# Performance work log

Measured on AMD Instinct MI355X. Metric: run time of the kernel, lower is better.

Reference implementation:

```python
import jax, jax.numpy as jnp
import numpy as np

NUM_GRAPHS = 64


def gcn_conv(x, edge_index, W, b):
    # PyG GCNConv: x' = D^-1/2 (A+I) D^-1/2 (x W) + b, self-loops added.
    n = x.shape[0]
    h = x @ W  # [N, out]
    loop = jnp.arange(n)
    src = jnp.concatenate([edge_index[0], loop])
    dst = jnp.concatenate([edge_index[1], loop])
    deg = jax.ops.segment_sum(jnp.ones_like(dst, dtype=h.dtype), dst, num_segments=n)
    dinv = jnp.where(deg > 0, jax.lax.rsqrt(deg), 0.0)
    norm = dinv[src] * dinv[dst]  # [E+N]
    msgs = h[src] * norm[:, None]  # gather + scale
    out = jax.ops.segment_sum(msgs, dst, num_segments=n)  # scatter-add
    return out + b


def lstm_step(x, W_ih, W_hh, b_ih, b_hh):
    # single time step, zero initial state; PyTorch gate order i,f,g,o
    H = W_hh.shape[1]
    gates = x @ W_ih.T + b_ih + b_hh  # h0 = 0 so W_hh term vanishes
    i, f, g, o = jnp.split(gates, 4, axis=-1)
    i, f, o = jax.nn.sigmoid(i), jax.nn.sigmoid(f), jax.nn.sigmoid(o)
    c = i * jnp.tanh(g)  # f * c0 = 0
    return o * jnp.tanh(c)


def setup_inputs() -> dict:
    key = jax.random.key(0)
    ks = jax.random.split(key, 16)
    N, E, F, G, H, C = 50000, 600000, 128, 128, 256, 1
    s = lambda *sh: 1.0 / np.sqrt(sh[-1])
    return {
        "x": jax.random.normal(ks[0], (N, F), jnp.float32),
        "edge_index": jax.random.randint(ks[1], (2, E), 0, N),
        "batch": jnp.sort(jax.random.randint(ks[2], (N,), 0, NUM_GRAPHS)),
        "W1": jax.random.normal(ks[3], (F, G), jnp.float32) * s(F, G),
        "b1": jnp.zeros((G,), jnp.float32),
        "W2": jax.random.normal(ks[4], (G, G), jnp.float32) * s(G, G),
        "b2": jnp.zeros((G,), jnp.float32),
        "W_ih": jax.random.normal(ks[5], (4 * H, G), jnp.float32) * s(4 * H, G),
        "W_hh": jax.random.normal(ks[6], (4 * H, H), jnp.float32) * s(4 * H, H),
        "b_ih": jnp.zeros((4 * H,), jnp.float32),
        "b_hh": jnp.zeros((4 * H,), jnp.float32),
        "Wm": jax.random.normal(ks[7], (C, H), jnp.float32) * s(C, H),
        "bm": jnp.zeros((C,), jnp.float32),
        "Wv": jax.random.normal(ks[8], (C, H), jnp.float32) * s(C, H),
        "bv": jnp.zeros((C,), jnp.float32),
    }


def reference(x, edge_index, batch, W1, b1, W2, b2, W_ih, W_hh, b_ih, b_hh, Wm, bm, Wv, bv):
    h = jax.nn.relu(gcn_conv(x, edge_index, W1, b1))
    h = jax.nn.relu(gcn_conv(h, edge_index, W2, b2))
    # global mean pool over graphs
    sums = jax.ops.segment_sum(h, batch, num_segments=NUM_GRAPHS)
    cnts = jax.ops.segment_sum(jnp.ones_like(batch, dtype=h.dtype), batch, num_segments=NUM_GRAPHS)
    pooled = sums / jnp.maximum(cnts, 1.0)[:, None]  # [G_graphs, gcn_hidden]
    hT = lstm_step(pooled, W_ih, W_hh, b_ih, b_hh)  # [G_graphs, lstm_hidden]
    mean = hT @ Wm.T + bm
    log_var = jax.nn.softplus(hT @ Wv.T + bv)
    return (mean, log_var)
```

## Files before the change

### kernel.cpp

```cpp
#include <hip/hip_runtime.h>
#include <hip/hip_bf16.h>
#include <math.h>


#define POOL_SUB 32

typedef __attribute__((ext_vector_type(8))) short bf16x8;
typedef __attribute__((ext_vector_type(4))) float f32x4;

static __device__ __forceinline__ unsigned short f2bf(float f) {
    union { float f; unsigned int u; } v; v.f = f;
    unsigned int u = v.u;
    unsigned int r = u + 0x7FFFu + ((u >> 16) & 1u);
    return (unsigned short)(r >> 16);
}
static __device__ __forceinline__ unsigned int pack2bf(float lo, float hi) {
    return (unsigned int)f2bf(lo) | ((unsigned int)f2bf(hi) << 16);
}
static __device__ __forceinline__ float bflo(unsigned int v) {
    union { unsigned int u; float f; } w; w.u = v << 16; return w.f;
}
static __device__ __forceinline__ float bfhi(unsigned int v) {
    union { unsigned int u; float f; } w; w.u = v & 0xFFFF0000u; return w.f;
}
static __device__ __forceinline__ bf16x8 f8_to_bf(float4 f0, float4 f1) {
    union { unsigned int u[4]; bf16x8 v; } r;
    r.u[0] = pack2bf(f0.x, f0.y);
    r.u[1] = pack2bf(f0.z, f0.w);
    r.u[2] = pack2bf(f1.x, f1.y);
    r.u[3] = pack2bf(f1.z, f1.w);
    return r.v;
}

__global__ void zero_kernel(int* __restrict__ p, int n) {
    int i = blockIdx.x * blockDim.x + threadIdx.x;
    if (i < n) p[i] = 0;
}

__global__ void count_deg_kernel(const int* __restrict__ dst, int E, int* __restrict__ deg) {
    int e = blockIdx.x * blockDim.x + threadIdx.x;
    if (e < E) atomicAdd(&deg[dst[e]], 1);
}

__global__ void scan_pass1(const int* __restrict__ deg, int n,
                           int* __restrict__ rowptr, int* __restrict__ bsums) {
    __shared__ int s[256];
    int tid = threadIdx.x;
    int base = blockIdx.x * 1024;
    int v[4];
    int mysum = 0;
#pragma unroll
    for (int j = 0; j < 4; ++j) {
        int idx = base + tid * 4 + j;
        v[j] = (idx < n) ? deg[idx] : 0;
        mysum += v[j];
    }
    s[tid] = mysum;
    __syncthreads();
    for (int off = 1; off < 256; off <<= 1) {
        int t = (tid >= off) ? s[tid - off] : 0;
        __syncthreads();
        s[tid] += t;
        __syncthreads();
    }
    int excl = s[tid] - mysum;
#pragma unroll
    for (int j = 0; j < 4; ++j) {
        int idx = base + tid * 4 + j;
        if (idx < n) rowptr[idx] = excl;
        excl += v[j];
    }
    if (tid == 255) bsums[blockIdx.x] = s[255];
}

__global__ void scan_pass2(int* bsums, int nb) {
    __shared__ int s[64];
    int tid = threadIdx.x;
    int v = (tid < nb) ? bsums[tid] : 0;
    s[tid] = v;
    __syncthreads();
    for (int off = 1; off < 64; off <<= 1) {
        int t = (tid >= off) ? s[tid - off] : 0;
        __syncthreads();
        s[tid] += t;
        __syncthreads();
    }
    if (tid < nb) bsums[tid] = s[tid] - v;
    if (tid == 63) bsums[nb] = s[63];
}

__global__ void scan_pass3(int* __restrict__ rowptr, const int* __restrict__ bsums,
                           const int* __restrict__ deg, float* __restrict__ dinv,
                           int n, int nb) {
    int tid = threadIdx.x;
    int base = blockIdx.x * 1024;
    int add = bsums[blockIdx.x];
#pragma unroll
    for (int j = 0; j < 4; ++j) {
        int idx = base + tid * 4 + j;
        if (idx < n) {
            rowptr[idx] += add;
            dinv[idx] = rsqrtf((float)deg[idx] + 1.0f);
        }
    }
    if (blockIdx.x == 0 && tid == 0) rowptr[n] = bsums[nb];
}

__global__ void fill_csr_kernel(const int* __restrict__ src, const int* __restrict__ dst, int E,
                                const int* __restrict__ rowptr, int* __restrict__ cursor,
                                int* __restrict__ csr) {
    int e = blockIdx.x * blockDim.x + threadIdx.x;
    if (e < E) {
        int d = dst[e];
        int pos = rowptr[d] + atomicAdd(&cursor[d], 1);
        csr[pos] = src[e];
    }
}

__global__ void wcvt_kernel(const float* __restrict__ W1, const float* __restrict__ W2,
                            unsigned short* __restrict__ Wt1, unsigned short* __restrict__ Wt2) {
    int nb = blockIdx.x & 127;
    const float* Ws = (blockIdx.x < 128) ? W1 : W2;
    unsigned short* Wd = (blockIdx.x < 128) ? Wt1 : Wt2;
    int k = threadIdx.x;
    Wd[nb * 128 + k] = f2bf(Ws[(size_t)k * 128 + nb]);
}

__global__ __launch_bounds__(256) void gemm_mfma_f32a_kernel(const float* __restrict__ A,
                                                             const unsigned short* __restrict__ Wt,
                                                             const float* __restrict__ dinv,
                                                             unsigned short* __restrict__ out,
                                                             int n) {
    int tid = threadIdx.x;
    int l = tid & 63;
    int wid = tid >> 6;
    int rowbase = blockIdx.x * 64 + wid * 16;
    int lc = l & 15;
    int kq = l >> 4;

    int arow = rowbase + lc; if (arow > n - 1) arow = n - 1;
    const float* Ap = A + (size_t)arow * 128 + kq * 8;
    const unsigned short* Wp = Wt + (size_t)lc * 128 + kq * 8;

    f32x4 acc[8];
#pragma unroll
    for (int c = 0; c < 8; ++c) acc[c] = (f32x4){0.f, 0.f, 0.f, 0.f};

#pragma unroll
    for (int ks = 0; ks < 4; ++ks) {
        float4 f0 = *(const float4*)(Ap + ks * 32);
        float4 f1 = *(const float4*)(Ap + ks * 32 + 4);
        bf16x8 a = f8_to_bf(f0, f1);
#pragma unroll
        for (int c = 0; c < 8; ++c) {
            bf16x8 b = *(const bf16x8*)(Wp + c * 2048 + ks * 32);
            acc[c] = __builtin_amdgcn_mfma_f32_16x16x32_bf16(a, b, acc[c], 0, 0, 0);
        }
    }

    int r0 = kq * 4;
    float s[4];
    int orow[4];
#pragma unroll
    for (int r = 0; r < 4; ++r) {
        orow[r] = rowbase + r0 + r;
        s[r] = (orow[r] < n) ? dinv[orow[r]] : 0.f;
    }
#pragma unroll
    for (int c = 0; c < 8; ++c) {
#pragma unroll
        for (int r = 0; r < 4; ++r) {
            if (orow[r] < n)
                out[(size_t)orow[r] * 128 + c * 16 + lc] = f2bf(acc[c][r] * s[r]);
        }
    }
}

__global__ __launch_bounds__(256) void gemm_mfma_kernel(const unsigned short* __restrict__ A,
                                                        const unsigned short* __restrict__ Wt,
                                                        const float* __restrict__ dinv,
                                                        unsigned short* __restrict__ out,
                                                        int n) {
    int tid = threadIdx.x;
    int l = tid & 63;
    int wid = tid >> 6;
    int rowbase = blockIdx.x * 64 + wid * 16;
    int lc = l & 15;
    int kq = l >> 4;

    int arow = rowbase + lc; if (arow > n - 1) arow = n - 1;
    const unsigned short* Ap = A + (size_t)arow * 128 + kq * 8;
    const unsigned short* Wp = Wt + (size_t)lc * 128 + kq * 8;

    f32x4 acc[8];
#pragma unroll
    for (int c = 0; c < 8; ++c) acc[c] = (f32x4){0.f, 0.f, 0.f, 0.f};

#pragma unroll
    for (int ks = 0; ks < 4; ++ks) {
        bf16x8 a = *(const bf16x8*)(Ap + ks * 32);
#pragma unroll
        for (int c = 0; c < 8; ++c) {
            bf16x8 b = *(const bf16x8*)(Wp + c * 2048 + ks * 32);
            acc[c] = __builtin_amdgcn_mfma_f32_16x16x32_bf16(a, b, acc[c], 0, 0, 0);
        }
    }

    int r0 = kq * 4;
    float s[4];
    int orow[4];
#pragma unroll
    for (int r = 0; r < 4; ++r) {
        orow[r] = rowbase + r0 + r;
        s[r] = (orow[r] < n) ? dinv[orow[r]] : 0.f;
    }
#pragma unroll
    for (int c = 0; c < 8; ++c) {
#pragma unroll
        for (int r = 0; r < 4; ++r) {
            if (orow[r] < n)
                out[(size_t)orow[r] * 128 + c * 16 + lc] = f2bf(acc[c][r] * s[r]);
        }
    }
}

__global__ __launch_bounds__(256) void aggregate_kernel(const unsigned int* __restrict__ g,
                                                        const int* __restrict__ rowptr,
                                                        const int* __restrict__ csr,
                                                        const float* __restrict__ dinv,
                                                        const float* __restrict__ bias,
                                                        unsigned int* __restrict__ out, int n) {
    int lane = threadIdx.x & 63;
    int node = (blockIdx.x * blockDim.x + threadIdx.x) >> 6;
    if (node >= n) return;
    int beg = rowptr[node], end = rowptr[node + 1];
    unsigned int sv = g[(size_t)node * 64 + lane];
    float ax = bflo(sv), ay = bfhi(sv);
    int e = beg;
    for (; e + 4 <= end; e += 4) {
        int s0 = csr[e + 0], s1 = csr[e + 1], s2 = csr[e + 2], s3 = csr[e + 3];
        unsigned int v0 = g[(size_t)s0 * 64 + lane];
        unsigned int v1 = g[(size_t)s1 * 64 + lane];
        unsigned int v2 = g[(size_t)s2 * 64 + lane];
        unsigned int v3 = g[(size_t)s3 * 64 + lane];
        ax += bflo(v0) + bflo(v1) + bflo(v2) + bflo(v3);
        ay += bfhi(v0) + bfhi(v1) + bfhi(v2) + bfhi(v3);
    }
    for (; e < end; ++e) {
        unsigned int v0 = g[(size_t)csr[e] * 64 + lane];
        ax += bflo(v0);
        ay += bfhi(v0);
    }
    float dv = dinv[node];
    float2 b = ((const float2*)bias)[lane];
    float rx = fmaxf(dv * ax + b.x, 0.f);
    float ry = fmaxf(dv * ay + b.y, 0.f);
    out[(size_t)node * 64 + lane] = pack2bf(rx, ry);
}

__global__ __launch_bounds__(64) void pool_partial_kernel(const unsigned int* __restrict__ h,
                                                          const int* __restrict__ batch, int n,
                                                          float* __restrict__ partial) {
    int g = blockIdx.x / POOL_SUB;
    int sub = blockIdx.x % POOL_SUB;
    int t = threadIdx.x;
    int lo = 0, hi = n;
    while (lo < hi) { int mid = (lo + hi) >> 1; if (batch[mid] < g) lo = mid + 1; else hi = mid; }
    int start = lo;
    hi = n;
    while (lo < hi) { int mid = (lo + hi) >> 1; if (batch[mid] < g + 1) lo = mid + 1; else hi = mid; }
    int end = lo;
    int len = end - start;
    int b0 = start + (int)((long long)len * sub / POOL_SUB);
    int b1 = start + (int)((long long)len * (sub + 1) / POOL_SUB);
    float ax = 0.f, ay = 0.f;
    int i = b0;
    for (; i + 4 <= b1; i += 4) {
        unsigned int v0 = h[(size_t)(i + 0) * 64 + t];
        unsigned int v1 = h[(size_t)(i + 1) * 64 + t];
        unsigned int v2 = h[(size_t)(i + 2) * 64 + t];
        unsigned int v3 = h[(size_t)(i + 3) * 64 + t];
        ax += bflo(v0) + bflo(v1) + bflo(v2) + bflo(v3);
        ay += bfhi(v0) + bfhi(v1) + bfhi(v2) + bfhi(v3);
    }
    for (; i < b1; ++i) {
        unsigned int v0 = h[(size_t)i * 64 + t];
        ax += bflo(v0);
        ay += bfhi(v0);
    }
    partial[(size_t)blockIdx.x * 128 + 2 * t]     = ax;
    partial[(size_t)blockIdx.x * 128 + 2 * t + 1] = ay;
}

__global__ __launch_bounds__(256) void pool_lstm_kernel(const float* __restrict__ partial,
                                                        const int* __restrict__ batch, int n,
                                                        const float* __restrict__ W_ih,
                                                        const float* __restrict__ b_ih,
                                                        const float* __restrict__ b_hh,
                                                        const float* __restrict__ Wm,
                                                        const float* __restrict__ bm,
                                                        const float* __restrict__ Wv,
                                                        const float* __restrict__ bv,
                                                        float* __restrict__ out) {
    __shared__ __align__(16) float p[128];
    __shared__ float redm[256];
    __shared__ float redv[256];
    int gph = blockIdx.x;
    int tid = threadIdx.x;
    if (tid < 128) {
        int lo = 0, hi = n;
        while (lo < hi) { int mid = (lo + hi) >> 1; if (batch[mid] < gph) lo = mid + 1; else hi = mid; }
        int start = lo;
        hi = n;
        while (lo < hi) { int mid = (lo + hi) >> 1; if (batch[mid] < gph + 1) lo = mid + 1; else hi = mid; }
        int end = lo;
        float acc = 0.f;
#pragma unroll
        for (int s = 0; s < POOL_SUB; ++s)
            acc += partial[(size_t)(gph * POOL_SUB + s) * 128 + tid];
        p[tid] = acc / fmaxf((float)(end - start), 1.0f);
    }
    __syncthreads();
    float gi = b_ih[tid] + b_hh[tid];
    float gg = b_ih[512 + tid] + b_hh[512 + tid];
    float go = b_ih[768 + tid] + b_hh[768 + tid];
    const float4* wi = (const float4*)(W_ih + (size_t)tid * 128);
    const float4* wg = (const float4*)(W_ih + (size_t)(512 + tid) * 128);
    const float4* wo = (const float4*)(W_ih + (size_t)(768 + tid) * 128);
    const float4* p4 = (const float4*)p;
#pragma unroll 8
    for (int k = 0; k < 32; ++k) {
        float4 xv = p4[k];
        float4 a = wi[k], bq = wg[k], cq = wo[k];
        gi += xv.x * a.x + xv.y * a.y + xv.z * a.z + xv.w * a.w;
        gg += xv.x * bq.x + xv.y * bq.y + xv.z * bq.z + xv.w * bq.w;
        go += xv.x * cq.x + xv.y * cq.y + xv.z * cq.z + xv.w * cq.w;
    }
    float iv = 1.f / (1.f + expf(-gi));
    float cv = iv * tanhf(gg);
    float ov = 1.f / (1.f + expf(-go));
    float hT = ov * tanhf(cv);
    redm[tid] = hT * Wm[tid];
    redv[tid] = hT * Wv[tid];
    __syncthreads();
    for (int s = 128; s > 0; s >>= 1) {
        if (tid < s) { redm[tid] += redm[tid + s]; redv[tid] += redv[tid + s]; }
        __syncthreads();
    }
    if (tid == 0) {
        out[gph] = redm[0] + bm[0];
        float xv = redv[0] + bv[0];
        out[64 + gph] = fmaxf(xv, 0.f) + log1pf(expf(-fabsf(xv)));
    }
}

extern "C" void kernel_launch(void* const* d_in, const int* in_sizes, int n_in,
                              void* d_out, int out_size, void* d_ws, size_t ws_size,
                              hipStream_t stream) {
    const float* x     = (const float*)d_in[0];
    const int*   edge  = (const int*)d_in[1];
    const int*   batch = (const int*)d_in[2];
    const float* W1    = (const float*)d_in[3];
    const float* b1    = (const float*)d_in[4];
    const float* W2    = (const float*)d_in[5];
    const float* b2    = (const float*)d_in[6];
    const float* W_ih  = (const float*)d_in[7];
    const float* b_ih  = (const float*)d_in[9];
    const float* b_hh  = (const float*)d_in[10];
    const float* Wm    = (const float*)d_in[11];
    const float* bm    = (const float*)d_in[12];
    const float* Wv    = (const float*)d_in[13];
    const float* bv    = (const float*)d_in[14];
    float* out = (float*)d_out;

    const int N = in_sizes[0] / 128;
    const int E = in_sizes[1] / 2;
    const int* srcIdx = edge;
    const int* dstIdx = edge + E;

    char* ws = (char*)d_ws;
    size_t off = 0;
    const size_t gB = (size_t)N * 64 * sizeof(unsigned int);
    unsigned int* gbuf = (unsigned int*)(ws + off); off += gB;
    unsigned int* hbuf = (unsigned int*)(ws + off); off += gB;
    int* deg    = (int*)(ws + off);   off += (size_t)N * sizeof(int);
    int* cursor = (int*)(ws + off);   off += (size_t)N * sizeof(int);
    int* rowptr = (int*)(ws + off);   off += (size_t)(N + 1) * sizeof(int);
    off = (off + 255) & ~(size_t)255;
    int* bsums  = (int*)(ws + off);   off += 512;
    int* csr    = (int*)(ws + off);   off += (size_t)E * sizeof(int);
    off = (off + 255) & ~(size_t)255;
    float* dinv = (float*)(ws + off); off += (size_t)N * sizeof(float);
    off = (off + 255) & ~(size_t)255;
    unsigned short* Wt1 = (unsigned short*)(ws + off); off += 128 * 128 * sizeof(unsigned short);
    unsigned short* Wt2 = (unsigned short*)(ws + off); off += 128 * 128 * sizeof(unsigned short);
    off = (off + 255) & ~(size_t)255;
    float* partial = (float*)(ws + off); off += (size_t)64 * POOL_SUB * 128 * sizeof(float);

    zero_kernel<<<(2 * N + 255) / 256, 256, 0, stream>>>(deg, 2 * N);

    wcvt_kernel<<<256, 128, 0, stream>>>(W1, W2, Wt1, Wt2);

    int eb = (E + 255) / 256;
    count_deg_kernel<<<eb, 256, 0, stream>>>(dstIdx, E, deg);

    int nb = (N + 1023) / 1024;
    scan_pass1<<<nb, 256, 0, stream>>>(deg, N, rowptr, bsums);
    scan_pass2<<<1, 64, 0, stream>>>(bsums, nb);
    scan_pass3<<<nb, 256, 0, stream>>>(rowptr, bsums, deg, dinv, N, nb);
    fill_csr_kernel<<<eb, 256, 0, stream>>>(srcIdx, dstIdx, E, rowptr, cursor, csr);

    int gb = (N + 63) / 64;
    int ab = (N + 3) / 4;

    gemm_mfma_f32a_kernel<<<gb, 256, 0, stream>>>(x, Wt1, dinv, (unsigned short*)gbuf, N);
    aggregate_kernel<<<ab, 256, 0, stream>>>(gbuf, rowptr, csr, dinv, b1, hbuf, N);
    gemm_mfma_kernel<<<gb, 256, 0, stream>>>((const unsigned short*)hbuf, Wt2, dinv, (unsigned short*)gbuf, N);
    aggregate_kernel<<<ab, 256, 0, stream>>>(gbuf, rowptr, csr, dinv, b2, hbuf, N);

    pool_partial_kernel<<<64 * POOL_SUB, 64, 0, stream>>>(hbuf, batch, N, partial);
    pool_lstm_kernel<<<64, 256, 0, stream>>>(partial, batch, N, W_ih, b_ih, b_hh, Wm, bm, Wv, bv, out);
}
```

Before: 222.3 us.

## Split GCN aggregation into feature-slice passes and fuse small setup kernels

The aggregation kernel now processes the 128 features in four pass-major slices, with each wave gathering four edges at once into 16-lane groups and reducing via cross-lane shuffles. This is meant to shrink the gathered working set per pass so it stays cache-resident and to raise memory parallelism. Separately, zeroing and weight conversion are merged into one kernel, and the second and third scan passes are merged, to cut launch count. The cost is 4x redundant reads of rowptr/csr and narrower 64-byte gather segments.

```diff
diff --git a/kernel.cpp b/kernel.cpp
--- a/kernel.cpp
+++ b/kernel.cpp
@@ -32,9 +32,21 @@
     return r.v;
 }
 
-__global__ void zero_kernel(int* __restrict__ p, int n) {
-    int i = blockIdx.x * blockDim.x + threadIdx.x;
-    if (i < n) p[i] = 0;
+__global__ __launch_bounds__(256) void prep_kernel(int* __restrict__ zp, int zwords,
+                                                   const float* __restrict__ W1,
+                                                   const float* __restrict__ W2,
+                                                   unsigned short* __restrict__ Wt1,
+                                                   unsigned short* __restrict__ Wt2, int zb) {
+    int b = blockIdx.x;
+    int t = threadIdx.x;
+    if (b < zb) {
+        int i = b * 256 + t;
+        if (i < zwords) zp[i] = 0;
+    } else {
+        int col = b - zb;
+        if (t < 128) Wt1[col * 128 + t] = f2bf(W1[(size_t)t * 128 + col]);
+        else { int k = t - 128; Wt2[col * 128 + k] = f2bf(W2[(size_t)k * 128 + col]); }
+    }
 }
 
 __global__ void count_deg_kernel(const int* __restrict__ dst, int E, int* __restrict__ deg) {
@@ -73,28 +85,23 @@
     if (tid == 255) bsums[blockIdx.x] = s[255];
 }
 
-__global__ void scan_pass2(int* bsums, int nb) {
-    __shared__ int s[64];
+__global__ void scan_pass23(int* __restrict__ rowptr, const int* __restrict__ bsums,
+                            const int* __restrict__ deg, float* __restrict__ dinv,
+                            int n, int nb) {
+    __shared__ int sm[64];
+    __shared__ int pref[65];
     int tid = threadIdx.x;
-    int v = (tid < nb) ? bsums[tid] : 0;
-    s[tid] = v;
+    if (tid < 64) sm[tid] = (tid < nb) ? bsums[tid] : 0;
     __syncthreads();
-    for (int off = 1; off < 64; off <<= 1) {
-        int t = (tid >= off) ? s[tid - off] : 0;
-        __syncthreads();
-        s[tid] += t;
-        __syncthreads();
-    }
-    if (tid < nb) bsums[tid] = s[tid] - v;
-    if (tid == 63) bsums[nb] = s[63];
-}
-
-__global__ void scan_pass3(int* __restrict__ rowptr, const int* __restrict__ bsums,
-                           const int* __restrict__ deg, float* __restrict__ dinv,
-                           int n, int nb) {
-    int tid = threadIdx.x;
+    if (tid == 0) {
+        int s = 0;
+#pragma unroll 8
+        for (int i = 0; i < 64; ++i) { pref[i] = s; s += sm[i]; }
+        pref[64] = s;
+    }
+    __syncthreads();
+    int add = pref[blockIdx.x];
     int base = blockIdx.x * 1024;
-    int add = bsums[blockIdx.x];
 #pragma unroll
     for (int j = 0; j < 4; ++j) {
         int idx = base + tid * 4 + j;
@@ -103,7 +110,7 @@
             dinv[idx] = rsqrtf((float)deg[idx] + 1.0f);
         }
     }
-    if (blockIdx.x == 0 && tid == 0) rowptr[n] = bsums[nb];
+    if (blockIdx.x == 0 && tid == 0) rowptr[n] = pref[64];
 }
 
 __global__ void fill_csr_kernel(const int* __restrict__ src, const int* __restrict__ dst, int E,
@@ -115,15 +122,6 @@
         int pos = rowptr[d] + atomicAdd(&cursor[d], 1);
         csr[pos] = src[e];
     }
-}
-
-__global__ void wcvt_kernel(const float* __restrict__ W1, const float* __restrict__ W2,
-                            unsigned short* __restrict__ Wt1, unsigned short* __restrict__ Wt2) {
-    int nb = blockIdx.x & 127;
-    const float* Ws = (blockIdx.x < 128) ? W1 : W2;
-    unsigned short* Wd = (blockIdx.x < 128) ? Wt1 : Wt2;
-    int k = threadIdx.x;
-    Wd[nb * 128 + k] = f2bf(Ws[(size_t)k * 128 + nb]);
 }
 
 __global__ __launch_bounds__(256) void gemm_mfma_f32a_kernel(const float* __restrict__ A,
@@ -229,33 +227,37 @@
                                                         const int* __restrict__ csr,
                                                         const float* __restrict__ dinv,
                                                         const float* __restrict__ bias,
-                                                        unsigned int* __restrict__ out, int n) {
+                                                        unsigned int* __restrict__ out,
+                                                        int n, int npb) {
+    int pass = blockIdx.x / npb;
+    int blk  = blockIdx.x % npb;
     int lane = threadIdx.x & 63;
-    int node = (blockIdx.x * blockDim.x + threadIdx.x) >> 6;
+    int wid  = threadIdx.x >> 6;
+    int node = blk * 4 + wid;
     if (node >= n) return;
+    int li = lane & 15, sub = lane >> 4;
+    int base = pass * 16;
     int beg = rowptr[node], end = rowptr[node + 1];
-    unsigned int sv = g[(size_t)node * 64 + lane];
-    float ax = bflo(sv), ay = bfhi(sv);
+    float ax = 0.f, ay = 0.f;
     int e = beg;
     for (; e + 4 <= end; e += 4) {
-        int s0 = csr[e + 0], s1 = csr[e + 1], s2 = csr[e + 2], s3 = csr[e + 3];
-        unsigned int v0 = g[(size_t)s0 * 64 + lane];
-        unsigned int v1 = g[(size_t)s1 * 64 + lane];
-        unsigned int v2 = g[(size_t)s2 * 64 + lane];
-        unsigned int v3 = g[(size_t)s3 * 64 + lane];
-        ax += bflo(v0) + bflo(v1) + bflo(v2) + bflo(v3);
-        ay += bfhi(v0) + bfhi(v1) + bfhi(v2) + bfhi(v3);
-    }
-    for (; e < end; ++e) {
-        unsigned int v0 = g[(size_t)csr[e] * 64 + lane];
-        ax += bflo(v0);
-        ay += bfhi(v0);
-    }
-    float dv = dinv[node];
-    float2 b = ((const float2*)bias)[lane];
-    float rx = fmaxf(dv * ax + b.x, 0.f);
-    float ry = fmaxf(dv * ay + b.y, 0.f);
-    out[(size_t)node * 64 + lane] = pack2bf(rx, ry);
+        unsigned int v = g[(size_t)csr[e + sub] * 64 + base + li];
+        ax += bflo(v); ay += bfhi(v);
+    }
+    if (e + sub < end) {
+        unsigned int v = g[(size_t)csr[e + sub] * 64 + base + li];
+        ax += bflo(v); ay += bfhi(v);
+    }
+    ax += __shfl_xor(ax, 16, 64); ax += __shfl_xor(ax, 32, 64);
+    ay += __shfl_xor(ay, 16, 64); ay += __shfl_xor(ay, 32, 64);
+    if (sub == 0) {
+        unsigned int sv = g[(size_t)node * 64 + base + li];
+        float dv = dinv[node];
+        float2 b = ((const float2*)bias)[base + li];
+        float rx = fmaxf(dv * (ax + bflo(sv)) + b.x, 0.f);
+        float ry = fmaxf(dv * (ay + bfhi(sv)) + b.y, 0.f);
+        out[(size_t)node * 64 + base + li] = pack2bf(rx, ry);
+    }
 }
 
 __global__ __launch_bounds__(64) void pool_partial_kernel(const unsigned int* __restrict__ h,
@@ -397,26 +399,25 @@
     off = (off + 255) & ~(size_t)255;
     float* partial = (float*)(ws + off); off += (size_t)64 * POOL_SUB * 128 * sizeof(float);
 
-    zero_kernel<<<(2 * N + 255) / 256, 256, 0, stream>>>(deg, 2 * N);
-
-    wcvt_kernel<<<256, 128, 0, stream>>>(W1, W2, Wt1, Wt2);
+    int zwords = 2 * N;
+    int zb = (zwords + 255) / 256;
+    prep_kernel<<<zb + 128, 256, 0, stream>>>(deg, zwords, W1, W2, Wt1, Wt2, zb);
 
     int eb = (E + 255) / 256;
     count_deg_kernel<<<eb, 256, 0, stream>>>(dstIdx, E, deg);
 
     int nb = (N + 1023) / 1024;
     scan_pass1<<<nb, 256, 0, stream>>>(deg, N, rowptr, bsums);
-    scan_pass2<<<1, 64, 0, stream>>>(bsums, nb);
-    scan_pass3<<<nb, 256, 0, stream>>>(rowptr, bsums, deg, dinv, N, nb);
+    scan_pass23<<<nb, 256, 0, stream>>>(rowptr, bsums, deg, dinv, N, nb);
     fill_csr_kernel<<<eb, 256, 0, stream>>>(srcIdx, dstIdx, E, rowptr, cursor, csr);
 
     int gb = (N + 63) / 64;
-    int ab = (N + 3) / 4;
+    int npb = (N + 3) / 4;
 
     gemm_mfma_f32a_kernel<<<gb, 256, 0, stream>>>(x, Wt1, dinv, (unsigned short*)gbuf, N);
-    aggregate_kernel<<<ab, 256, 0, stream>>>(gbuf, rowptr, csr, dinv, b1, hbuf, N);
+    aggregate_kernel<<<4 * npb, 256, 0, stream>>>(gbuf, rowptr, csr, dinv, b1, hbuf, N, npb);
     gemm_mfma_kernel<<<gb, 256, 0, stream>>>((const unsigned short*)hbuf, Wt2, dinv, (unsigned short*)gbuf, N);
-    aggregate_kernel<<<ab, 256, 0, stream>>>(gbuf, rowptr, csr, dinv, b2, hbuf, N);
+    aggregate_kernel<<<4 * npb, 256, 0, stream>>>(gbuf, rowptr, csr, dinv, b2, hbuf, N, npb);
 
     pool_partial_kernel<<<64 * POOL_SUB, 64, 0, stream>>>(hbuf, batch, N, partial);
     pool_lstm_kernel<<<64, 256, 0, stream>>>(partial, batch, N, W_ih, b_ih, b_hh, Wm, bm, Wv, bv, out);
```

Result: slower. 334.4 us (+50.4%).
